# Kernel tuning notes

Measured on AMD Instinct MI355X. Metric: run time of the kernel, lower is better.

Reference implementation:

```python
import jax, jax.numpy as jnp
import numpy as np

B, T, C, H = 4, 2048, 768, 12
D = C // H


def setup_inputs() -> dict:
    key = jax.random.key(0)
    ks = jax.random.split(key, 7)
    s = 0.02
    return {
        "q": jax.random.normal(ks[0], (B, T, C), jnp.float32),
        "k": jax.random.normal(ks[1], (B, T, C), jnp.float32),
        "v": jax.random.normal(ks[2], (B, T, C), jnp.float32),
        "w_q": jax.random.normal(ks[3], (C, C), jnp.float32) * s,
        "w_k": jax.random.normal(ks[4], (C, C), jnp.float32) * s,
        "w_v": jax.random.normal(ks[5], (C, C), jnp.float32) * s,
        "w_o": jax.random.normal(ks[6], (C, C), jnp.float32) * s,
    }


def reference(q, k, v, w_q, w_k, w_v, w_o):
    # Linear projections (torch Linear: x @ W^T, bias=False)
    qh = (q @ w_q.T).reshape(B, T, H, D).transpose(0, 2, 1, 3)  # [B,H,T,D]
    kh = (k @ w_k.T).reshape(B, T, H, D).transpose(0, 2, 1, 3)
    vh = (v @ w_v.T).reshape(B, T, H, D).transpose(0, 2, 1, 3)
    scale = 1.0 / jnp.sqrt(jnp.asarray(D, qh.dtype))
    att = jnp.einsum("bhqd,bhkd->bhqk", qh, kh) * scale  # [B,H,T,T]
    causal = jnp.tril(jnp.ones((T, T), bool))
    att = jnp.where(causal[None, None], att, -jnp.inf)
    att = jax.nn.softmax(att, axis=-1)
    y = jnp.einsum("bhqk,bhkd->bhqd", att, vh)  # [B,H,T,D]
    y = y.transpose(0, 2, 1, 3).reshape(B, T, C)
    return y @ w_o.T
```

## Files before the change

### kernel.cpp

```cpp
#include <hip/hip_runtime.h>

#define BB 4
#define TT 2048
#define CC 768
#define HH 12
#define DD 64
#define MM (BB * TT)

#define QSCALE 0.18033688011112042f

typedef __attribute__((ext_vector_type(8))) __bf16 bf16x8;
typedef __attribute__((ext_vector_type(4))) __bf16 bf16x4;
typedef __attribute__((ext_vector_type(4))) float f32x4;

__device__ inline void gload16(const void* g, void* l) {
  __builtin_amdgcn_global_load_lds(
      (const __attribute__((address_space(1))) unsigned int*)g,
      (__attribute__((address_space(3))) unsigned int*)l, 16, 0, 0);
}

__device__ inline void cast_body(const float* __restrict__ s, __bf16* __restrict__ d) {
  long i = ((long)blockIdx.x * 256 + threadIdx.x) * 8;
  f32x4 a = *(const f32x4*)(s + i);
  f32x4 b = *(const f32x4*)(s + i + 4);
  bf16x8 o;
  o[0] = (__bf16)a[0]; o[1] = (__bf16)a[1]; o[2] = (__bf16)a[2]; o[3] = (__bf16)a[3];
  o[4] = (__bf16)b[0]; o[5] = (__bf16)b[1]; o[6] = (__bf16)b[2]; o[7] = (__bf16)b[3];
  *(bf16x8*)(d + i) = o;
}

__global__ __launch_bounds__(256) void cast3(const float* __restrict__ s0, const float* __restrict__ s1,
                                             const float* __restrict__ s2,
                                             __bf16* d0, __bf16* d1, __bf16* d2) {
  const float* s = blockIdx.y == 0 ? s0 : blockIdx.y == 1 ? s1 : s2;
  __bf16* d = blockIdx.y == 0 ? d0 : blockIdx.y == 1 ? d1 : d2;
  cast_body(s, d);
}

__global__ __launch_bounds__(256) void cast4(const float* __restrict__ s0, const float* __restrict__ s1,
                                             const float* __restrict__ s2, const float* __restrict__ s3,
                                             __bf16* d0, __bf16* d1, __bf16* d2, __bf16* d3) {
  const float* s; __bf16* d;
  switch (blockIdx.y) {
    case 0: s = s0; d = d0; break;
    case 1: s = s1; d = d1; break;
    case 2: s = s2; d = d2; break;
    default: s = s3; d = d3; break;
  }
  cast_body(s, d);
}

template <int MODE>
__global__ __launch_bounds__(256) void gemm_proj(
    const __bf16* __restrict__ A0, const __bf16* __restrict__ A1, const __bf16* __restrict__ A2,
    const __bf16* __restrict__ W0, const __bf16* __restrict__ W1, const __bf16* __restrict__ W2,
    void* D0, void* D1, void* D2) {
  __shared__ __bf16 As[128 * 64];
  __shared__ __bf16 Bs[128 * 64];
  const int z = blockIdx.z;
  const __bf16* __restrict__ A = z == 0 ? A0 : z == 1 ? A1 : A2;
  const __bf16* __restrict__ W = z == 0 ? W0 : z == 1 ? W1 : W2;
  const int m0 = blockIdx.y * 128;
  const int n0 = blockIdx.x * 128;
  const int tid = threadIdx.x;
  const int wave = tid >> 6, lane = tid & 63;
  const int l15 = lane & 15, g = lane >> 4;
  const int wr = (wave >> 1) * 64, wc = (wave & 1) * 64;

  f32x4 acc[4][4] = {};

  for (int kt = 0; kt < CC / 64; ++kt) {
    __syncthreads();
    const int k0 = kt * 64;
#pragma unroll
    for (int i = 0; i < 4; ++i) {
      const int r = wave + i * 4;
      const int L = r * 1024 + lane * 16;
      const int row = L >> 7;
      const int sc = (L >> 4) & 7;
      const int gc = sc ^ (row & 7);
      gload16(A + (long)(m0 + row) * CC + k0 + gc * 8, &As[r * 512]);
      gload16(W + (long)(n0 + row) * CC + k0 + gc * 8, &Bs[r * 512]);
    }
    __syncthreads();

#pragma unroll
    for (int kk = 0; kk < 2; ++kk) {
      bf16x8 af[4], bfr[4];
#pragma unroll
      for (int mi = 0; mi < 4; ++mi) {
        const int row = wr + mi * 16 + l15;
        const int c = (kk * 4 + g) ^ (row & 7);
        af[mi] = *(const bf16x8*)&As[row * 64 + c * 8];
      }
#pragma unroll
      for (int ni = 0; ni < 4; ++ni) {
        const int row = wc + ni * 16 + l15;
        const int c = (kk * 4 + g) ^ (row & 7);
        bfr[ni] = *(const bf16x8*)&Bs[row * 64 + c * 8];
      }
#pragma unroll
      for (int mi = 0; mi < 4; ++mi)
#pragma unroll
        for (int ni = 0; ni < 4; ++ni)
          acc[mi][ni] = __builtin_amdgcn_mfma_f32_16x16x32_bf16(af[mi], bfr[ni], acc[mi][ni], 0, 0, 0);
    }
  }

#pragma unroll
  for (int mi = 0; mi < 4; ++mi) {
#pragma unroll
    for (int ni = 0; ni < 4; ++ni) {
#pragma unroll
      for (int j = 0; j < 4; ++j) {
        const int m = m0 + wr + mi * 16 + g * 4 + j;
        const int n = n0 + wc + ni * 16 + l15;
        float v = acc[mi][ni][j];
        if (MODE == 0) {
          __bf16* Dst = (__bf16*)(z == 0 ? D0 : z == 1 ? D1 : D2);
          const int b = m >> 11, t = m & (TT - 1), h = n >> 6, d = n & 63;
          if (z == 0) v *= QSCALE;
          if (z == 2)
            Dst[(((long)(b * HH + h)) * DD + d) * TT + t] = (__bf16)v;
          else
            Dst[(((long)(b * HH + h)) * TT + t) * DD + d] = (__bf16)v;
        } else {
          float* Dst = (float*)D0;
          Dst[(long)m * CC + n] = v;
        }
      }
    }
  }
}

__global__ __launch_bounds__(256) void attn_fwd(
    const __bf16* __restrict__ Qh, const __bf16* __restrict__ Kh,
    const __bf16* __restrict__ Vh, __bf16* __restrict__ Y) {
  __shared__ __bf16 Kl[2][64 * 64];
  __shared__ __bf16 Vl[2][64 * 64];
  __shared__ __bf16 Pl[4][16 * 72];

  const int bh = blockIdx.y;
  const int a = blockIdx.x;
  const int tid = threadIdx.x, wave = tid >> 6, lane = tid & 63;
  const int l15 = lane & 15, g = lane >> 4;
  const __bf16* Kbase = Kh + (long)bh * TT * DD;
  const __bf16* VTbase = Vh + (long)bh * DD * TT;
  const int b = bh / HH, h = bh % HH;

  const int s_a = a + 1;
  const int total = 33;

  int qt = a;
  int qrow = qt * 64 + wave * 16 + l15;
  bf16x8 qf0, qf1;
  {
    const __bf16* qptr = Qh + ((long)bh * TT + qrow) * DD;
    qf0 = *(const bf16x8*)(qptr + g * 8);
    qf1 = *(const bf16x8*)(qptr + 32 + g * 8);
  }

  f32x4 oacc[4] = {};
  float m = -1e30f, lsum = 0.f;

#pragma unroll
  for (int i = 0; i < 2; ++i) {
    const int r = wave + i * 4;
    const int L = r * 1024 + lane * 16;
    const int row = L >> 7, sc = (L >> 4) & 7, gc = sc ^ (row & 7);
    gload16(Kbase + (long)row * DD + gc * 8, &Kl[0][r * 512]);
    gload16(VTbase + (long)row * TT + gc * 8, &Vl[0][r * 512]);
  }

  for (int s = 0; s < total; ++s) {
    __syncthreads();

    if (s + 1 < total) {
      const int kt1 = (s + 1 >= s_a) ? (s + 1 - s_a) : (s + 1);
      const int kv1 = kt1 * 64;
      __bf16* Kd = Kl[(s + 1) & 1];
      __bf16* Vd = Vl[(s + 1) & 1];
#pragma unroll
      for (int i = 0; i < 2; ++i) {
        const int r = wave + i * 4;
        const int L = r * 1024 + lane * 16;
        const int row = L >> 7, sc = (L >> 4) & 7, gc = sc ^ (row & 7);
        gload16(Kbase + (long)(kv1 + row) * DD + gc * 8, Kd + r * 512);
        gload16(VTbase + (long)row * TT + kv1 + gc * 8, Vd + r * 512);
      }
    }

    if (s == s_a) {
#pragma unroll
      for (int j = 0; j < 4; ++j) {
        const float lq = __shfl(lsum, g * 4 + j);
        const float inv = 1.0f / lq;
        const int q = qt * 64 + wave * 16 + g * 4 + j;
#pragma unroll
        for (int ni = 0; ni < 4; ++ni)
          Y[((long)(b * TT + q)) * CC + h * DD + ni * 16 + l15] = (__bf16)(oacc[ni][j] * inv);
      }
      qt = 31 - a;
      qrow = qt * 64 + wave * 16 + l15;
      const __bf16* qptr = Qh + ((long)bh * TT + qrow) * DD;
      qf0 = *(const bf16x8*)(qptr + g * 8);
      qf1 = *(const bf16x8*)(qptr + 32 + g * 8);
#pragma unroll
      for (int ni = 0; ni < 4; ++ni) oacc[ni] = (f32x4){0.f, 0.f, 0.f, 0.f};
      m = -1e30f; lsum = 0.f;
    }

    const int kt = (s >= s_a) ? (s - s_a) : s;
    const int kv0 = kt * 64;
    const bool maskt = (kt == qt);
    const __bf16* Kc = Kl[s & 1];
    const __bf16* Vc = Vl[s & 1];

    f32x4 sacc[4] = {};
#pragma unroll
    for (int mi = 0; mi < 4; ++mi) {
      const int row = mi * 16 + l15;
      const int c0 = g ^ (row & 7);
      const int c1 = (4 + g) ^ (row & 7);
      bf16x8 kfa = *(const bf16x8*)&Kc[row * 64 + c0 * 8];
      bf16x8 kfb = *(const bf16x8*)&Kc[row * 64 + c1 * 8];
      sacc[mi] = __builtin_amdgcn_mfma_f32_16x16x32_bf16(kfa, qf0, sacc[mi], 0, 0, 0);
      sacc[mi] = __builtin_amdgcn_mfma_f32_16x16x32_bf16(kfb, qf1, sacc[mi], 0, 0, 0);
    }

    float ps[4][4];
    float tmax = -1e30f;
#pragma unroll
    for (int mi = 0; mi < 4; ++mi) {
#pragma unroll
      for (int j = 0; j < 4; ++j) {
        float sv = sacc[mi][j];
        const int kv = kv0 + mi * 16 + g * 4 + j;
        if (maskt && kv > qrow) sv = -1e30f;
        ps[mi][j] = sv;
        tmax = fmaxf(tmax, sv);
      }
    }
    tmax = fmaxf(tmax, __shfl_xor(tmax, 16));
    tmax = fmaxf(tmax, __shfl_xor(tmax, 32));

    if (!__all(tmax <= m + 8.0f)) {
      const float mnew = fmaxf(m, tmax);
      const float corr = exp2f(m - mnew);
#pragma unroll
      for (int j = 0; j < 4; ++j) {
        const float cj = __shfl(corr, g * 4 + j);
#pragma unroll
        for (int ni = 0; ni < 4; ++ni) oacc[ni][j] *= cj;
      }
      lsum *= corr;
      m = mnew;
    }

    float rsum = 0.f;
#pragma unroll
    for (int mi = 0; mi < 4; ++mi) {
      bf16x4 pv;
#pragma unroll
      for (int j = 0; j < 4; ++j) {
        const float p = exp2f(ps[mi][j] - m);
        rsum += p;
        pv[j] = (__bf16)p;
      }
      *(bf16x4*)&Pl[wave][l15 * 72 + mi * 16 + g * 4] = pv;
    }
    rsum += __shfl_xor(rsum, 16);
    rsum += __shfl_xor(rsum, 32);
    lsum += rsum;

#pragma unroll
    for (int ks = 0; ks < 2; ++ks) {
      bf16x8 pa = *(const bf16x8*)&Pl[wave][l15 * 72 + ks * 32 + g * 8];
#pragma unroll
      for (int ni = 0; ni < 4; ++ni) {
        const int d = ni * 16 + l15;
        const int c = (ks * 4 + g) ^ (d & 7);
        bf16x8 vf = *(const bf16x8*)&Vc[d * 64 + c * 8];
        oacc[ni] = __builtin_amdgcn_mfma_f32_16x16x32_bf16(pa, vf, oacc[ni], 0, 0, 0);
      }
    }
  }

#pragma unroll
  for (int j = 0; j < 4; ++j) {
    const float lq = __shfl(lsum, g * 4 + j);
    const float inv = 1.0f / lq;
    const int q = qt * 64 + wave * 16 + g * 4 + j;
#pragma unroll
    for (int ni = 0; ni < 4; ++ni)
      Y[((long)(b * TT + q)) * CC + h * DD + ni * 16 + l15] = (__bf16)(oacc[ni][j] * inv);
  }
}

extern "C" void kernel_launch(void* const* d_in, const int* in_sizes, int n_in,
                              void* d_out, int out_size, void* d_ws, size_t ws_size,
                              hipStream_t stream) {
  (void)in_sizes; (void)n_in; (void)out_size; (void)ws_size;
  const float* q  = (const float*)d_in[0];
  const float* k  = (const float*)d_in[1];
  const float* v  = (const float*)d_in[2];
  const float* wq = (const float*)d_in[3];
  const float* wk = (const float*)d_in[4];
  const float* wv = (const float*)d_in[5];
  const float* wo = (const float*)d_in[6];

  char* ws = (char*)d_ws;
  const long SZX = (long)MM * CC * 2;
  const long SZW = (long)CC * CC * 2;
  __bf16* xq  = (__bf16*)(ws);
  __bf16* xk  = (__bf16*)(ws + SZX);
  __bf16* xv  = (__bf16*)(ws + 2 * SZX);
  __bf16* wwq = (__bf16*)(ws + 3 * SZX);
  __bf16* wwk = (__bf16*)(ws + 3 * SZX + SZW);
  __bf16* wwv = (__bf16*)(ws + 3 * SZX + 2 * SZW);
  __bf16* wwo = (__bf16*)(ws + 3 * SZX + 3 * SZW);
  __bf16* qh  = (__bf16*)(ws + 3 * SZX + 4 * SZW);
  __bf16* kh  = (__bf16*)(ws + 4 * SZX + 4 * SZW);
  __bf16* vh  = (__bf16*)(ws + 5 * SZX + 4 * SZW);
  __bf16* y   = xq;

  cast3<<<dim3((MM * CC) / 2048, 3, 1), 256, 0, stream>>>(q, k, v, xq, xk, xv);
  cast4<<<dim3((CC * CC) / 2048, 4, 1), 256, 0, stream>>>(wq, wk, wv, wo, wwq, wwk, wwv, wwo);
  gemm_proj<0><<<dim3(CC / 128, MM / 128, 3), 256, 0, stream>>>(xq, xk, xv, wwq, wwk, wwv, qh, kh, vh);
  attn_fwd<<<dim3(TT / 128, BB * HH, 1), 256, 0, stream>>>(qh, kh, vh, y);
  gemm_proj<1><<<dim3(CC / 128, MM / 128, 1), 256, 0, stream>>>(y, y, y, wwo, wwo, wwo, d_out, d_out, d_out);
}
```

Measured before the change: 287.2 us.

## Double-buffer GEMM K loop, stage epilogue via LDS, trim attention softmax reductions

The projection GEMM now uses two LDS buffers so the next K tile's global-to-LDS load overlaps MFMA work on the current tile. Its epilogue goes through swizzled shared memory, so output is written as 16-byte vector stores (transposed for V) instead of scattered scalar stores. In attention, the per-tile row-sum shuffle reduction is deferred to the end, the max reduction runs only when the rescale branch fires, unmasked tiles skip the mask check, and the P buffer uses XOR swizzling instead of padding. The 64 KB of LDS per GEMM block may lower occupancy.

```diff
diff --git a/kernel.cpp b/kernel.cpp
--- a/kernel.cpp
+++ b/kernel.cpp
@@ -50,18 +50,62 @@
   cast_body(s, d);
 }
 
+__device__ inline void stage_tile(const __bf16* __restrict__ A, const __bf16* __restrict__ W,
+                                  long m0, long n0, int k0,
+                                  __bf16* As, __bf16* Bs, int wave, int lane) {
+#pragma unroll
+  for (int i = 0; i < 4; ++i) {
+    const int r = wave + i * 4;
+    const int L = r * 1024 + lane * 16;
+    const int row = L >> 7;
+    const int sc = (L >> 4) & 7;
+    const int gc = sc ^ (row & 7);
+    gload16(A + (m0 + row) * CC + k0 + gc * 8, As + r * 512);
+    gload16(W + (n0 + row) * CC + k0 + gc * 8, Bs + r * 512);
+  }
+}
+
+__device__ inline void compute_tile(const __bf16* As, const __bf16* Bs, f32x4 (&acc)[4][4],
+                                    int wr, int wc, int l15, int g) {
+#pragma unroll
+  for (int kk = 0; kk < 2; ++kk) {
+    bf16x8 af[4], bfr[4];
+#pragma unroll
+    for (int mi = 0; mi < 4; ++mi) {
+      const int row = wr + mi * 16 + l15;
+      const int c = (kk * 4 + g) ^ (row & 7);
+      af[mi] = *(const bf16x8*)&As[row * 64 + c * 8];
+    }
+#pragma unroll
+    for (int ni = 0; ni < 4; ++ni) {
+      const int row = wc + ni * 16 + l15;
+      const int c = (kk * 4 + g) ^ (row & 7);
+      bfr[ni] = *(const bf16x8*)&Bs[row * 64 + c * 8];
+    }
+#pragma unroll
+    for (int mi = 0; mi < 4; ++mi)
+#pragma unroll
+      for (int ni = 0; ni < 4; ++ni)
+        acc[mi][ni] = __builtin_amdgcn_mfma_f32_16x16x32_bf16(af[mi], bfr[ni], acc[mi][ni], 0, 0, 0);
+  }
+}
+
 template <int MODE>
 __global__ __launch_bounds__(256) void gemm_proj(
     const __bf16* __restrict__ A0, const __bf16* __restrict__ A1, const __bf16* __restrict__ A2,
     const __bf16* __restrict__ W0, const __bf16* __restrict__ W1, const __bf16* __restrict__ W2,
     void* D0, void* D1, void* D2) {
-  __shared__ __bf16 As[128 * 64];
-  __shared__ __bf16 Bs[128 * 64];
+  __shared__ __align__(16) char smem[65536];
+  __bf16* As0 = (__bf16*)smem;
+  __bf16* Bs0 = (__bf16*)(smem + 16384);
+  __bf16* As1 = (__bf16*)(smem + 32768);
+  __bf16* Bs1 = (__bf16*)(smem + 49152);
+
   const int z = blockIdx.z;
   const __bf16* __restrict__ A = z == 0 ? A0 : z == 1 ? A1 : A2;
   const __bf16* __restrict__ W = z == 0 ? W0 : z == 1 ? W1 : W2;
-  const int m0 = blockIdx.y * 128;
-  const int n0 = blockIdx.x * 128;
+  const long m0 = blockIdx.y * 128;
+  const long n0 = blockIdx.x * 128;
   const int tid = threadIdx.x;
   const int wave = tid >> 6, lane = tid & 63;
   const int l15 = lane & 15, g = lane >> 4;
@@ -69,64 +113,95 @@
 
   f32x4 acc[4][4] = {};
 
-  for (int kt = 0; kt < CC / 64; ++kt) {
+  stage_tile(A, W, m0, n0, 0, As0, Bs0, wave, lane);
+  __syncthreads();
+  for (int kt = 0; kt < 12; kt += 2) {
+    stage_tile(A, W, m0, n0, (kt + 1) * 64, As1, Bs1, wave, lane);
+    compute_tile(As0, Bs0, acc, wr, wc, l15, g);
     __syncthreads();
-    const int k0 = kt * 64;
-#pragma unroll
-    for (int i = 0; i < 4; ++i) {
-      const int r = wave + i * 4;
-      const int L = r * 1024 + lane * 16;
-      const int row = L >> 7;
-      const int sc = (L >> 4) & 7;
-      const int gc = sc ^ (row & 7);
-      gload16(A + (long)(m0 + row) * CC + k0 + gc * 8, &As[r * 512]);
-      gload16(W + (long)(n0 + row) * CC + k0 + gc * 8, &Bs[r * 512]);
-    }
+    if (kt + 2 < 12) stage_tile(A, W, m0, n0, (kt + 2) * 64, As0, Bs0, wave, lane);
+    compute_tile(As1, Bs1, acc, wr, wc, l15, g);
     __syncthreads();
-
-#pragma unroll
-    for (int kk = 0; kk < 2; ++kk) {
-      bf16x8 af[4], bfr[4];
-#pragma unroll
-      for (int mi = 0; mi < 4; ++mi) {
-        const int row = wr + mi * 16 + l15;
-        const int c = (kk * 4 + g) ^ (row & 7);
-        af[mi] = *(const bf16x8*)&As[row * 64 + c * 8];
-      }
-#pragma unroll
-      for (int ni = 0; ni < 4; ++ni) {
-        const int row = wc + ni * 16 + l15;
-        const int c = (kk * 4 + g) ^ (row & 7);
-        bfr[ni] = *(const bf16x8*)&Bs[row * 64 + c * 8];
-      }
-#pragma unroll
-      for (int mi = 0; mi < 4; ++mi)
-#pragma unroll
-        for (int ni = 0; ni < 4; ++ni)
-          acc[mi][ni] = __builtin_amdgcn_mfma_f32_16x16x32_bf16(af[mi], bfr[ni], acc[mi][ni], 0, 0, 0);
-    }
-  }
-
-#pragma unroll
-  for (int mi = 0; mi < 4; ++mi) {
-#pragma unroll
-    for (int ni = 0; ni < 4; ++ni) {
-#pragma unroll
-      for (int j = 0; j < 4; ++j) {
-        const int m = m0 + wr + mi * 16 + g * 4 + j;
-        const int n = n0 + wc + ni * 16 + l15;
-        float v = acc[mi][ni][j];
-        if (MODE == 0) {
-          __bf16* Dst = (__bf16*)(z == 0 ? D0 : z == 1 ? D1 : D2);
-          const int b = m >> 11, t = m & (TT - 1), h = n >> 6, d = n & 63;
-          if (z == 0) v *= QSCALE;
-          if (z == 2)
-            Dst[(((long)(b * HH + h)) * DD + d) * TT + t] = (__bf16)v;
-          else
-            Dst[(((long)(b * HH + h)) * TT + t) * DD + d] = (__bf16)v;
+  }
+
+  const int b = (int)(m0 >> 11);
+  const int t0 = (int)(m0 & (TT - 1));
+  if (MODE == 1) {
+    float* Ef = (float*)smem;
+    float* Dst = (float*)D0;
+    for (int p = 0; p < 2; ++p) {
+      if (p) __syncthreads();
+      if ((wr >> 6) == p) {
+#pragma unroll
+        for (int mi = 0; mi < 4; ++mi)
+#pragma unroll
+          for (int ni = 0; ni < 4; ++ni)
+#pragma unroll
+            for (int j = 0; j < 4; ++j) {
+              const int ml = mi * 16 + g * 4 + j;
+              const int n = wc + ni * 16 + l15;
+              *(float*)((char*)Ef + ml * 512 + ((n * 4) ^ (((ml >> 2) & 7) << 4))) = acc[mi][ni][j];
+            }
+      }
+      __syncthreads();
+#pragma unroll
+      for (int sw = 0; sw < 8; ++sw) {
+        const int r = sw * 8 + (tid >> 5);
+        const int c = (tid & 31) * 4;
+        f32x4 vv = *(const f32x4*)((char*)Ef + r * 512 + ((c * 4) ^ (((r >> 2) & 7) << 4)));
+        *(f32x4*)&Dst[(m0 + p * 64 + r) * CC + n0 + c] = vv;
+      }
+    }
+  } else {
+    __bf16* Eh = (__bf16*)smem;
+    __bf16* Dst = (__bf16*)(z == 0 ? D0 : z == 1 ? D1 : D2);
+    for (int p = 0; p < 2; ++p) {
+      if (p) __syncthreads();
+      if (z != 2) {
+        if ((wr >> 6) == p) {
+#pragma unroll
+          for (int mi = 0; mi < 4; ++mi)
+#pragma unroll
+            for (int ni = 0; ni < 4; ++ni)
+#pragma unroll
+              for (int j = 0; j < 4; ++j) {
+                const int ml = mi * 16 + g * 4 + j;
+                const int n = wc + ni * 16 + l15;
+                float v = acc[mi][ni][j];
+                if (z == 0) v *= QSCALE;
+                *(__bf16*)((char*)Eh + ml * 256 + ((n * 2) ^ (((ml >> 2) & 7) << 4))) = (__bf16)v;
+              }
+        }
+      } else {
+        if ((wc >> 6) == p) {
+#pragma unroll
+          for (int mi = 0; mi < 4; ++mi)
+#pragma unroll
+            for (int ni = 0; ni < 4; ++ni)
+#pragma unroll
+              for (int j = 0; j < 4; ++j) {
+                const int nl = ni * 16 + l15;
+                const int mm = wr + mi * 16 + g * 4 + j;
+                *(__bf16*)((char*)Eh + nl * 256 + ((mm * 2) ^ ((nl & 7) << 4))) = (__bf16)acc[mi][ni][j];
+              }
+        }
+      }
+      __syncthreads();
+#pragma unroll
+      for (int sw = 0; sw < 4; ++sw) {
+        const int r = sw * 16 + (tid >> 4);
+        const int c = (tid & 15) * 8;
+        if (z != 2) {
+          bf16x8 vv = *(const bf16x8*)((char*)Eh + r * 256 + ((c * 2) ^ (((r >> 2) & 7) << 4)));
+          const int t = t0 + p * 64 + r;
+          const int n = (int)n0 + c;
+          const int h = n >> 6, d = n & 63;
+          *(bf16x8*)&Dst[(((long)(b * HH + h)) * TT + t) * DD + d] = vv;
         } else {
-          float* Dst = (float*)D0;
-          Dst[(long)m * CC + n] = v;
+          bf16x8 vv = *(const bf16x8*)((char*)Eh + r * 256 + ((c * 2) ^ ((r & 7) << 4)));
+          const int n = (int)n0 + p * 64 + r;
+          const int h = n >> 6, d = n & 63;
+          *(bf16x8*)&Dst[(((long)(b * HH + h)) * DD + d) * TT + t0 + c] = vv;
         }
       }
     }
@@ -138,7 +213,7 @@
     const __bf16* __restrict__ Vh, __bf16* __restrict__ Y) {
   __shared__ __bf16 Kl[2][64 * 64];
   __shared__ __bf16 Vl[2][64 * 64];
-  __shared__ __bf16 Pl[4][16 * 72];
+  __shared__ __bf16 Pl[4][16 * 64];
 
   const int bh = blockIdx.y;
   const int a = blockIdx.x;
@@ -147,6 +222,7 @@
   const __bf16* Kbase = Kh + (long)bh * TT * DD;
   const __bf16* VTbase = Vh + (long)bh * DD * TT;
   const int b = bh / HH, h = bh % HH;
+  char* Pb = (char*)&Pl[wave][0];
 
   const int s_a = a + 1;
   const int total = 33;
@@ -191,10 +267,11 @@
     }
 
     if (s == s_a) {
+      float lrow = lsum + __shfl_xor(lsum, 16);
+      lrow += __shfl_xor(lrow, 32);
 #pragma unroll
       for (int j = 0; j < 4; ++j) {
-        const float lq = __shfl(lsum, g * 4 + j);
-        const float inv = 1.0f / lq;
+        const float inv = 1.0f / __shfl(lrow, g * 4 + j);
         const int q = qt * 64 + wave * 16 + g * 4 + j;
 #pragma unroll
         for (int ni = 0; ni < 4; ++ni)
@@ -229,23 +306,33 @@
     }
 
     float ps[4][4];
-    float tmax = -1e30f;
-#pragma unroll
-    for (int mi = 0; mi < 4; ++mi) {
-#pragma unroll
-      for (int j = 0; j < 4; ++j) {
-        float sv = sacc[mi][j];
-        const int kv = kv0 + mi * 16 + g * 4 + j;
-        if (maskt && kv > qrow) sv = -1e30f;
-        ps[mi][j] = sv;
-        tmax = fmaxf(tmax, sv);
-      }
-    }
-    tmax = fmaxf(tmax, __shfl_xor(tmax, 16));
-    tmax = fmaxf(tmax, __shfl_xor(tmax, 32));
+    float tmax = -3e30f;
+    if (maskt) {
+#pragma unroll
+      for (int mi = 0; mi < 4; ++mi)
+#pragma unroll
+        for (int j = 0; j < 4; ++j) {
+          float sv = sacc[mi][j];
+          const int kv = kv0 + mi * 16 + g * 4 + j;
+          if (kv > qrow) sv = -3e30f;
+          ps[mi][j] = sv;
+          tmax = fmaxf(tmax, sv);
+        }
+    } else {
+#pragma unroll
+      for (int mi = 0; mi < 4; ++mi)
+#pragma unroll
+        for (int j = 0; j < 4; ++j) {
+          const float sv = sacc[mi][j];
+          ps[mi][j] = sv;
+          tmax = fmaxf(tmax, sv);
+        }
+    }
 
     if (!__all(tmax <= m + 8.0f)) {
-      const float mnew = fmaxf(m, tmax);
+      float full = fmaxf(tmax, __shfl_xor(tmax, 16));
+      full = fmaxf(full, __shfl_xor(full, 32));
+      const float mnew = fmaxf(m, full);
       const float corr = exp2f(m - mnew);
 #pragma unroll
       for (int j = 0; j < 4; ++j) {
@@ -257,25 +344,21 @@
       m = mnew;
     }
 
-    float rsum = 0.f;
 #pragma unroll
     for (int mi = 0; mi < 4; ++mi) {
       bf16x4 pv;
 #pragma unroll
       for (int j = 0; j < 4; ++j) {
         const float p = exp2f(ps[mi][j] - m);
-        rsum += p;
+        lsum += p;
         pv[j] = (__bf16)p;
       }
-      *(bf16x4*)&Pl[wave][l15 * 72 + mi * 16 + g * 4] = pv;
-    }
-    rsum += __shfl_xor(rsum, 16);
-    rsum += __shfl_xor(rsum, 32);
-    lsum += rsum;
+      *(bf16x4*)(Pb + l15 * 128 + ((mi * 32 + g * 8) ^ ((l15 & 7) << 4))) = pv;
+    }
 
 #pragma unroll
     for (int ks = 0; ks < 2; ++ks) {
-      bf16x8 pa = *(const bf16x8*)&Pl[wave][l15 * 72 + ks * 32 + g * 8];
+      bf16x8 pa = *(const bf16x8*)(Pb + l15 * 128 + ((ks * 64 + g * 16) ^ ((l15 & 7) << 4)));
 #pragma unroll
       for (int ni = 0; ni < 4; ++ni) {
         const int d = ni * 16 + l15;
@@ -286,14 +369,17 @@
     }
   }
 
-#pragma unroll
-  for (int j = 0; j < 4; ++j) {
-    const float lq = __shfl(lsum, g * 4 + j);
-    const float inv = 1.0f / lq;
-    const int q = qt * 64 + wave * 16 + g * 4 + j;
-#pragma unroll
-    for (int ni = 0; ni < 4; ++ni)
-      Y[((long)(b * TT + q)) * CC + h * DD + ni * 16 + l15] = (__bf16)(oacc[ni][j] * inv);
+  {
+    float lrow = lsum + __shfl_xor(lsum, 16);
+    lrow += __shfl_xor(lrow, 32);
+#pragma unroll
+    for (int j = 0; j < 4; ++j) {
+      const float inv = 1.0f / __shfl(lrow, g * 4 + j);
+      const int q = qt * 64 + wave * 16 + g * 4 + j;
+#pragma unroll
+      for (int ni = 0; ni < 4; ++ni)
+        Y[((long)(b * TT + q)) * CC + h * DD + ni * 16 + l15] = (__bf16)(oacc[ni][j] * inv);
+    }
   }
 }
 
```

Measured after the change: 261.9 us. -8.8%, faster.
